# Optimization experiments

Measured on AMD Instinct MI355X. Metric: run time of the kernel, lower is better.

## Reference

```python
import jax, jax.numpy as jnp
import numpy as np

N_NODES = 100000

def gcn_conv(x, row, col, w, W, b, n):
    # PyG GCNConv with edge weights: add self-loops, symmetric normalization.
    loop = jnp.arange(n)
    r = jnp.concatenate([row, loop])
    c = jnp.concatenate([col, loop])
    ew = jnp.concatenate([w, jnp.ones((n,), dtype=x.dtype)])
    deg = jax.ops.segment_sum(ew, c, num_segments=n)          # [N]
    dinv = jnp.where(deg > 0, jax.lax.rsqrt(deg), 0.0)
    norm = dinv[r] * ew * dinv[c]                              # [E+N]
    h = x @ W                                                  # [N, C]
    msg = norm[:, None] * h[r]                                 # [E+N, C]
    out = jax.ops.segment_sum(msg, c, num_segments=n)          # [N, C]
    return out + b

def setup_inputs() -> dict:
    key = jax.random.key(0)
    ks = jax.random.split(key, 9)
    n, F, H, O = N_NODES, 128, 128, 64  # H = 2*out_channels
    E = 1600000
    x = jax.random.normal(ks[0], (n, F), dtype=jnp.float32)
    edge_index = jax.random.randint(ks[1], (2, E), 0, n, dtype=jnp.int64)
    edge_attr = jax.random.uniform(ks[2], (E,), dtype=jnp.float32)
    s = 1.0 / np.sqrt(F)
    W1 = jax.random.uniform(ks[3], (F, H), jnp.float32, -s, s)
    b1 = jnp.zeros((H,), jnp.float32)
    s2 = 1.0 / np.sqrt(H)
    Wmu = jax.random.uniform(ks[4], (H, O), jnp.float32, -s2, s2)
    bmu = jnp.zeros((O,), jnp.float32)
    Wls = jax.random.uniform(ks[5], (H, O), jnp.float32, -s2, s2)
    bls = jnp.zeros((O,), jnp.float32)
    return {"x": x, "edge_index": edge_index, "edge_attr": edge_attr,
            "W1": W1, "b1": b1, "Wmu": Wmu, "bmu": bmu, "Wls": Wls, "bls": bls}

def reference(x, edge_index, edge_attr, W1, b1, Wmu, bmu, Wls, bls):
    n = x.shape[0]
    row, col = edge_index[0], edge_index[1]
    h = jax.nn.relu(gcn_conv(x, row, col, edge_attr, W1, b1, n))
    mu = gcn_conv(h, row, col, edge_attr, Wmu, bmu, n)
    logstd = gcn_conv(h, row, col, edge_attr, Wls, bls, n)
    return (mu, logstd)
```

## Files before the change

### kernel.cpp

```cpp
#include <hip/hip_runtime.h>
#include <math.h>


#define SCAN_B 512

typedef __attribute__((ext_vector_type(8))) short bf16x8;
typedef __attribute__((ext_vector_type(4))) float f32x4;

__device__ __forceinline__ unsigned short f2bf_rne(float f) {
  unsigned int u = __float_as_uint(f);
  u += 0x7FFFu + ((u >> 16) & 1u);
  return (unsigned short)(u >> 16);
}

__device__ __forceinline__ float bf2f(unsigned short h) {
  return __uint_as_float(((unsigned int)h) << 16);
}

__device__ __forceinline__ unsigned int pack2(unsigned short a, unsigned short b) {
  return (unsigned int)a | ((unsigned int)b << 16);
}

__global__ void init_cnt(int* __restrict__ cnt, int n) {
  int i = blockIdx.x * blockDim.x + threadIdx.x;
  if (i < n) cnt[i] = 0;
}

__global__ void hist_rank(const int* __restrict__ col, int* __restrict__ cnt,
                          int* __restrict__ rank, int E) {
  int e = blockIdx.x * blockDim.x + threadIdx.x;
  if (e < E) rank[e] = atomicAdd(&cnt[col[e]], 1);
}

__global__ void scan_blocks(const int* __restrict__ in, int* __restrict__ out,
                            int* __restrict__ bsum, int n) {
  __shared__ int s[SCAN_B];
  int gid = blockIdx.x * SCAN_B + threadIdx.x;
  int v = (gid < n) ? in[gid] : 0;
  s[threadIdx.x] = v;
  __syncthreads();
  for (int off = 1; off < SCAN_B; off <<= 1) {
    int t = (threadIdx.x >= off) ? s[threadIdx.x - off] : 0;
    __syncthreads();
    s[threadIdx.x] += t;
    __syncthreads();
  }
  if (gid < n) out[gid] = s[threadIdx.x] - v;
  if (bsum && threadIdx.x == SCAN_B - 1) bsum[blockIdx.x] = s[SCAN_B - 1];
}

__global__ void add_offsets(int* __restrict__ row_ptr, const int* __restrict__ bsum_ex,
                            int n, int E) {
  int i = blockIdx.x * blockDim.x + threadIdx.x;
  if (i < n) row_ptr[i] += bsum_ex[i >> 9];
  if (i == 0) row_ptr[n] = E;
}

__global__ void scatter_edges(const int* __restrict__ row, const int* __restrict__ col,
                              const float* __restrict__ w,
                              const int* __restrict__ row_ptr,
                              const int* __restrict__ rank,
                              int2* __restrict__ csr, int E) {
  int e = blockIdx.x * blockDim.x + threadIdx.x;
  if (e >= E) return;
  int pos = row_ptr[col[e]] + rank[e];
  csr[pos] = make_int2(row[e], __float_as_int(w[e]));
}

__global__ void deg_dinv(const int* __restrict__ row_ptr, const int2* __restrict__ csr,
                         float* __restrict__ dinv, int n) {
  int i = blockIdx.x * blockDim.x + threadIdx.x;
  if (i >= n) return;
  float s = 1.0f;
  int end = row_ptr[i + 1];
  for (int p = row_ptr[i]; p < end; ++p) s += __int_as_float(csr[p].y);
  dinv[i] = 1.0f / sqrtf(s);
}

__global__ void prep_wt(const float* __restrict__ Wsrc,
                        unsigned short* __restrict__ wt_hi,
                        unsigned short* __restrict__ wt_lo) {
  int i = blockIdx.x * blockDim.x + threadIdx.x;
  if (i >= 128 * 128) return;
  int n = i & 127, k = i >> 7;
  float f = Wsrc[(size_t)k * 128 + n];
  unsigned short h = f2bf_rne(f);
  unsigned short l = f2bf_rne(f - bf2f(h));
  wt_hi[(size_t)n * 128 + k] = h;
  wt_lo[(size_t)n * 128 + k] = l;
}

__global__ void prep_wcat_t(const float* __restrict__ Wmu, const float* __restrict__ Wls,
                            const float* __restrict__ bmu, const float* __restrict__ bls,
                            unsigned short* __restrict__ wt_hi,
                            unsigned short* __restrict__ wt_lo,
                            float* __restrict__ bcat) {
  int i = blockIdx.x * blockDim.x + threadIdx.x;
  if (i >= 128 * 128) return;
  int n = i & 127, k = i >> 7;
  float f = (n < 64) ? Wmu[(size_t)k * 64 + n] : Wls[(size_t)k * 64 + (n - 64)];
  unsigned short h = f2bf_rne(f);
  unsigned short l = f2bf_rne(f - bf2f(h));
  wt_hi[(size_t)n * 128 + k] = h;
  wt_lo[(size_t)n * 128 + k] = l;
  if (i < 128) bcat[i] = (i < 64) ? bmu[i] : bls[i - 64];
}

__global__ __launch_bounds__(256) void gemm_mfma(
    const float* __restrict__ A,
    const unsigned short* __restrict__ WtHi, const unsigned short* __restrict__ WtLo,
    const float* __restrict__ bias, const float* __restrict__ rowscale,
    float* __restrict__ C0, float* __restrict__ C1,
    unsigned short* __restrict__ Cbf, int split, int M) {
  __shared__ uint4 sAhi[1024];
  __shared__ uint4 sAlo[1024];
  __shared__ uint4 sWhi[1024];
  __shared__ uint4 sWlo[1024];

  int tid = threadIdx.x;
  int lane = tid & 63, wid = tid >> 6;
  int wave_r = (wid >> 1) * 64, wave_c = (wid & 1) * 64;
  int lrow = lane & 15, lkb = lane >> 4;
  int rowBase = blockIdx.x * 128;

  f32x4 acc[4][4];
#pragma unroll
  for (int mr = 0; mr < 4; ++mr)
#pragma unroll
    for (int nc = 0; nc < 4; ++nc) acc[mr][nc] = (f32x4){0.f, 0.f, 0.f, 0.f};

  const uint4* WtHi4 = (const uint4*)WtHi;
  const uint4* WtLo4 = (const uint4*)WtLo;

  for (int kt = 0; kt < 128; kt += 64) {
    __syncthreads();
#pragma unroll
    for (int j = 0; j < 4; ++j) {
      int g = tid + 256 * j;
      int c = g >> 3, k8 = g & 7;
      int slot = k8 ^ (c & 7);
      sWhi[c * 8 + slot] = WtHi4[c * 16 + (kt >> 3) + k8];
      sWlo[c * 8 + slot] = WtLo4[c * 16 + (kt >> 3) + k8];
    }
#pragma unroll
    for (int j = 0; j < 4; ++j) {
      int g = tid + 256 * j;
      int r = g >> 3, k8 = g & 7;
      int grow = rowBase + r;
      float4 v0 = make_float4(0.f, 0.f, 0.f, 0.f);
      float4 v1 = v0;
      if (grow < M) {
        const float4* Ar = (const float4*)(A + (size_t)grow * 128 + kt);
        v0 = Ar[k8 * 2];
        v1 = Ar[k8 * 2 + 1];
      }
      float f[8] = {v0.x, v0.y, v0.z, v0.w, v1.x, v1.y, v1.z, v1.w};
      unsigned short h[8], l[8];
#pragma unroll
      for (int q = 0; q < 8; ++q) {
        h[q] = f2bf_rne(f[q]);
        l[q] = f2bf_rne(f[q] - bf2f(h[q]));
      }
      int slot = k8 ^ (r & 7);
      sAhi[r * 8 + slot] = make_uint4(pack2(h[0], h[1]), pack2(h[2], h[3]),
                                      pack2(h[4], h[5]), pack2(h[6], h[7]));
      sAlo[r * 8 + slot] = make_uint4(pack2(l[0], l[1]), pack2(l[2], l[3]),
                                      pack2(l[4], l[5]), pack2(l[6], l[7]));
    }
    __syncthreads();
#pragma unroll
    for (int ks = 0; ks < 2; ++ks) {
      bf16x8 ah[4], al[4], bh[4], bl[4];
#pragma unroll
      for (int mr = 0; mr < 4; ++mr) {
        int r = wave_r + mr * 16 + lrow;
        int slot = (ks * 4 + lkb) ^ (r & 7);
        ah[mr] = *(const bf16x8*)&sAhi[r * 8 + slot];
        al[mr] = *(const bf16x8*)&sAlo[r * 8 + slot];
      }
#pragma unroll
      for (int nc = 0; nc < 4; ++nc) {
        int c = wave_c + nc * 16 + lrow;
        int slot = (ks * 4 + lkb) ^ (c & 7);
        bh[nc] = *(const bf16x8*)&sWhi[c * 8 + slot];
        bl[nc] = *(const bf16x8*)&sWlo[c * 8 + slot];
      }
#pragma unroll
      for (int mr = 0; mr < 4; ++mr)
#pragma unroll
        for (int nc = 0; nc < 4; ++nc) {
          acc[mr][nc] = __builtin_amdgcn_mfma_f32_16x16x32_bf16(
              ah[mr], bh[nc], acc[mr][nc], 0, 0, 0);
          acc[mr][nc] = __builtin_amdgcn_mfma_f32_16x16x32_bf16(
              al[mr], bh[nc], acc[mr][nc], 0, 0, 0);
          acc[mr][nc] = __builtin_amdgcn_mfma_f32_16x16x32_bf16(
              ah[mr], bl[nc], acc[mr][nc], 0, 0, 0);
        }
    }
  }

#pragma unroll
  for (int mr = 0; mr < 4; ++mr) {
    int Rb = rowBase + wave_r + mr * 16 + lkb * 4;
    float sc[4];
#pragma unroll
    for (int reg = 0; reg < 4; ++reg)
      sc[reg] = (rowscale && (Rb + reg) < M) ? rowscale[Rb + reg] : 1.0f;
#pragma unroll
    for (int nc = 0; nc < 4; ++nc) {
      int c = wave_c + nc * 16 + lrow;
      float bb = bias ? bias[c] : 0.f;
      f32x4 v = acc[mr][nc];
#pragma unroll
      for (int reg = 0; reg < 4; ++reg) {
        int R = Rb + reg;
        if (R >= M) continue;
        float val = v[reg] * sc[reg] + bb;
        if (Cbf) Cbf[(size_t)R * 128 + c] = f2bf_rne(val);
        if (C0) {
          if (c < split) C0[(size_t)R * split + c] = val;
          else           C1[(size_t)R * split + (c - split)] = val;
        }
      }
    }
  }
}

__global__ __launch_bounds__(256) void aggregate(
    const ushort4* __restrict__ hin, const int* __restrict__ row_ptr,
    const int2* __restrict__ csr, const float* __restrict__ dinv,
    const float4* __restrict__ bias4, ushort4* __restrict__ hout_bf,
    float4* __restrict__ hout_f4, int n, int do_relu, int scale_out) {
  int node = blockIdx.x * 8 + (threadIdx.x >> 5);
  if (node >= n) return;
  int t = threadIdx.x & 31;
  int beg = row_ptr[node], end = row_ptr[node + 1];
  ushort4 hs = hin[(size_t)node * 32 + t];
  float4 acc = make_float4(bf2f(hs.x), bf2f(hs.y), bf2f(hs.z), bf2f(hs.w));
  int p = beg;
  for (; p + 4 <= end; p += 4) {
    int2 e0 = csr[p + 0];
    int2 e1 = csr[p + 1];
    int2 e2 = csr[p + 2];
    int2 e3 = csr[p + 3];
    ushort4 h0 = hin[(size_t)e0.x * 32 + t];
    ushort4 h1 = hin[(size_t)e1.x * 32 + t];
    ushort4 h2 = hin[(size_t)e2.x * 32 + t];
    ushort4 h3 = hin[(size_t)e3.x * 32 + t];
    float w0 = __int_as_float(e0.y), w1 = __int_as_float(e1.y);
    float w2 = __int_as_float(e2.y), w3 = __int_as_float(e3.y);
    acc.x = fmaf(w0, bf2f(h0.x), acc.x); acc.y = fmaf(w0, bf2f(h0.y), acc.y);
    acc.z = fmaf(w0, bf2f(h0.z), acc.z); acc.w = fmaf(w0, bf2f(h0.w), acc.w);
    acc.x = fmaf(w1, bf2f(h1.x), acc.x); acc.y = fmaf(w1, bf2f(h1.y), acc.y);
    acc.z = fmaf(w1, bf2f(h1.z), acc.z); acc.w = fmaf(w1, bf2f(h1.w), acc.w);
    acc.x = fmaf(w2, bf2f(h2.x), acc.x); acc.y = fmaf(w2, bf2f(h2.y), acc.y);
    acc.z = fmaf(w2, bf2f(h2.z), acc.z); acc.w = fmaf(w2, bf2f(h2.w), acc.w);
    acc.x = fmaf(w3, bf2f(h3.x), acc.x); acc.y = fmaf(w3, bf2f(h3.y), acc.y);
    acc.z = fmaf(w3, bf2f(h3.z), acc.z); acc.w = fmaf(w3, bf2f(h3.w), acc.w);
  }
  for (; p < end; ++p) {
    int2 e = csr[p];
    ushort4 hv = hin[(size_t)e.x * 32 + t];
    float wv = __int_as_float(e.y);
    acc.x = fmaf(wv, bf2f(hv.x), acc.x); acc.y = fmaf(wv, bf2f(hv.y), acc.y);
    acc.z = fmaf(wv, bf2f(hv.z), acc.z); acc.w = fmaf(wv, bf2f(hv.w), acc.w);
  }
  float dc = dinv[node];
  float4 val = make_float4(dc * acc.x, dc * acc.y, dc * acc.z, dc * acc.w);
  if (bias4) {
    float4 b = bias4[t];
    val.x += b.x; val.y += b.y; val.z += b.z; val.w += b.w;
  }
  if (do_relu) {
    val.x = fmaxf(val.x, 0.f); val.y = fmaxf(val.y, 0.f);
    val.z = fmaxf(val.z, 0.f); val.w = fmaxf(val.w, 0.f);
  }
  if (scale_out) {
    val.x *= dc; val.y *= dc; val.z *= dc; val.w *= dc;
  }
  size_t o = (size_t)node * 32 + t;
  if (hout_bf) {
    ushort4 ov;
    ov.x = f2bf_rne(val.x); ov.y = f2bf_rne(val.y);
    ov.z = f2bf_rne(val.z); ov.w = f2bf_rne(val.w);
    hout_bf[o] = ov;
  }
  if (hout_f4) hout_f4[o] = val;
}

extern "C" void kernel_launch(void* const* d_in, const int* in_sizes, int n_in,
                              void* d_out, int out_size, void* d_ws, size_t ws_size,
                              hipStream_t stream) {
  const float* x   = (const float*)d_in[0];
  const int*   ei  = (const int*)d_in[1];
  const float* ea  = (const float*)d_in[2];
  const float* W1  = (const float*)d_in[3];
  const float* b1  = (const float*)d_in[4];
  const float* Wmu = (const float*)d_in[5];
  const float* bmu = (const float*)d_in[6];
  const float* Wls = (const float*)d_in[7];
  const float* bls = (const float*)d_in[8];
  const int N = in_sizes[0] / 128;
  const int E = in_sizes[2];
  const int* row = ei;
  const int* col = ei + E;

  char* p = (char*)d_ws;
  auto alloc = [&](size_t bytes) -> void* {
    void* r = (void*)p;
    p += (bytes + 255) & ~(size_t)255;
    return r;
  };
  float* dinv    = (float*)alloc((size_t)N * 4);
  int*   cnt     = (int*)alloc((size_t)N * 4);
  int*   row_ptr = (int*)alloc((size_t)(N + 1) * 4);
  int*   bsum    = (int*)alloc(1024 * 4);
  int*   bsum_ex = (int*)alloc(1024 * 4);
  unsigned short* w1t_hi = (unsigned short*)alloc(128 * 128 * 2);
  unsigned short* w1t_lo = (unsigned short*)alloc(128 * 128 * 2);
  unsigned short* wct_hi = (unsigned short*)alloc(128 * 128 * 2);
  unsigned short* wct_lo = (unsigned short*)alloc(128 * 128 * 2);
  float* bcat    = (float*)alloc(128 * 4);
  int2*  csr     = (int2*)alloc((size_t)E * 8);
  float* bufA    = (float*)alloc((size_t)N * 128 * 4);
  unsigned short* bufB = (unsigned short*)alloc((size_t)N * 128 * 2);
  unsigned short* bufC = (unsigned short*)alloc((size_t)N * 128 * 2);
  int*   rank    = (int*)bufA;

  float* out_mu = (float*)d_out;
  float* out_ls = out_mu + (size_t)N * 64;

  int nbN = (N + 255) / 256;
  int nbE = (E + 255) / 256;
  int NB  = (N + SCAN_B - 1) / SCAN_B;

  init_cnt<<<nbN, 256, 0, stream>>>(cnt, N);
  hist_rank<<<nbE, 256, 0, stream>>>(col, cnt, rank, E);
  prep_wt<<<64, 256, 0, stream>>>(W1, w1t_hi, w1t_lo);
  prep_wcat_t<<<64, 256, 0, stream>>>(Wmu, Wls, bmu, bls, wct_hi, wct_lo, bcat);
  scan_blocks<<<NB, SCAN_B, 0, stream>>>(cnt, row_ptr, bsum, N);
  scan_blocks<<<1, SCAN_B, 0, stream>>>(bsum, bsum_ex, nullptr, NB);
  add_offsets<<<nbN, 256, 0, stream>>>(row_ptr, bsum_ex, N, E);
  scatter_edges<<<nbE, 256, 0, stream>>>(row, col, ea, row_ptr, rank, csr, E);
  deg_dinv<<<nbN, 256, 0, stream>>>(row_ptr, csr, dinv, N);

  int gblocks = (N + 127) / 128;
  int ablocks = (N + 7) / 8;
  gemm_mfma<<<gblocks, 256, 0, stream>>>(x, w1t_hi, w1t_lo, nullptr, dinv,
                                         nullptr, nullptr, bufB, 128, N);
  aggregate<<<ablocks, 256, 0, stream>>>((const ushort4*)bufB, row_ptr, csr, dinv,
                                         (const float4*)b1, (ushort4*)bufC,
                                         nullptr, N, 1, 1);
  aggregate<<<ablocks, 256, 0, stream>>>((const ushort4*)bufC, row_ptr, csr, dinv,
                                         nullptr, nullptr, (float4*)bufA, N, 0, 0);
  gemm_mfma<<<gblocks, 256, 0, stream>>>(bufA, wct_hi, wct_lo, bcat, nullptr,
                                         out_mu, out_ls, nullptr, 64, N);
}
```

Baseline: 331.2 us.

## Build CSR via two-level bucket partition with shared-memory atomics

Replaces the global-atomic counting sort (per-edge atomicAdd on node counts, multi-level scan, random scatter) with a two-pass radix-style partition. Edges are first bucketed by col>>8 using shared-memory histograms and a per-block scan, then each bucket is sorted by its low 8 bits in a per-bucket kernel that writes row_ptr and the CSR. The goal is to avoid contended global atomics and the scattered global writes of the old path. In exchange it adds an extra pass over the edges and relies on N fitting in 17 bits and at most 512 buckets. Edge order within a node also becomes nondeterministic, which can change float summation order.

Result: faster. 283.6 us (-14.4%).

```diff
diff --git a/kernel.cpp b/kernel.cpp
--- a/kernel.cpp
+++ b/kernel.cpp
@@ -2,7 +2,7 @@
 #include <math.h>
 
 
-#define SCAN_B 512
+#define NBLK 1024
 
 typedef __attribute__((ext_vector_type(8))) short bf16x8;
 typedef __attribute__((ext_vector_type(4))) float f32x4;
@@ -21,50 +21,114 @@
   return (unsigned int)a | ((unsigned int)b << 16);
 }
 
-__global__ void init_cnt(int* __restrict__ cnt, int n) {
-  int i = blockIdx.x * blockDim.x + threadIdx.x;
-  if (i < n) cnt[i] = 0;
-}
-
-__global__ void hist_rank(const int* __restrict__ col, int* __restrict__ cnt,
-                          int* __restrict__ rank, int E) {
-  int e = blockIdx.x * blockDim.x + threadIdx.x;
-  if (e < E) rank[e] = atomicAdd(&cnt[col[e]], 1);
-}
-
-__global__ void scan_blocks(const int* __restrict__ in, int* __restrict__ out,
-                            int* __restrict__ bsum, int n) {
-  __shared__ int s[SCAN_B];
-  int gid = blockIdx.x * SCAN_B + threadIdx.x;
-  int v = (gid < n) ? in[gid] : 0;
+
+__global__ __launch_bounds__(256) void hist_coarse(const int* __restrict__ col,
+                                                   int* __restrict__ G,
+                                                   int E, int nbuck, int epb) {
+  __shared__ int h[512];
+  int blk = blockIdx.x;
+  for (int i = threadIdx.x; i < nbuck; i += 256) h[i] = 0;
+  __syncthreads();
+  int beg = blk * epb;
+  int end = min(beg + epb, E);
+  for (int p = beg + threadIdx.x; p < end; p += 256)
+    atomicAdd(&h[col[p] >> 8], 1);
+  __syncthreads();
+  for (int i = threadIdx.x; i < nbuck; i += 256)
+    G[(size_t)i * NBLK + blk] = h[i];
+}
+
+__global__ __launch_bounds__(1024) void scan_bucket(int* __restrict__ G,
+                                                    int* __restrict__ tot) {
+  __shared__ int s[NBLK];
+  int b = blockIdx.x;
+  int v = G[(size_t)b * NBLK + threadIdx.x];
   s[threadIdx.x] = v;
   __syncthreads();
-  for (int off = 1; off < SCAN_B; off <<= 1) {
+  for (int off = 1; off < NBLK; off <<= 1) {
     int t = (threadIdx.x >= off) ? s[threadIdx.x - off] : 0;
     __syncthreads();
     s[threadIdx.x] += t;
     __syncthreads();
   }
-  if (gid < n) out[gid] = s[threadIdx.x] - v;
-  if (bsum && threadIdx.x == SCAN_B - 1) bsum[blockIdx.x] = s[SCAN_B - 1];
-}
-
-__global__ void add_offsets(int* __restrict__ row_ptr, const int* __restrict__ bsum_ex,
-                            int n, int E) {
-  int i = blockIdx.x * blockDim.x + threadIdx.x;
-  if (i < n) row_ptr[i] += bsum_ex[i >> 9];
-  if (i == 0) row_ptr[n] = E;
-}
-
-__global__ void scatter_edges(const int* __restrict__ row, const int* __restrict__ col,
-                              const float* __restrict__ w,
-                              const int* __restrict__ row_ptr,
-                              const int* __restrict__ rank,
-                              int2* __restrict__ csr, int E) {
-  int e = blockIdx.x * blockDim.x + threadIdx.x;
-  if (e >= E) return;
-  int pos = row_ptr[col[e]] + rank[e];
-  csr[pos] = make_int2(row[e], __float_as_int(w[e]));
+  G[(size_t)b * NBLK + threadIdx.x] = s[threadIdx.x] - v;
+  if (threadIdx.x == NBLK - 1) tot[b] = s[NBLK - 1];
+}
+
+__global__ __launch_bounds__(512) void scan_start(const int* __restrict__ tot,
+                                                  int* __restrict__ start,
+                                                  int* __restrict__ row_ptr,
+                                                  int nbuck, int N, int E) {
+  __shared__ int s[512];
+  int v = (threadIdx.x < nbuck) ? tot[threadIdx.x] : 0;
+  s[threadIdx.x] = v;
+  __syncthreads();
+  for (int off = 1; off < 512; off <<= 1) {
+    int t = (threadIdx.x >= off) ? s[threadIdx.x - off] : 0;
+    __syncthreads();
+    s[threadIdx.x] += t;
+    __syncthreads();
+  }
+  if (threadIdx.x < nbuck) start[threadIdx.x] = s[threadIdx.x] - v;
+  if (threadIdx.x == 511) start[nbuck] = s[511];
+  if (threadIdx.x == 0) row_ptr[N] = E;
+}
+
+__global__ __launch_bounds__(256) void partition_edges(
+    const int* __restrict__ row, const int* __restrict__ col,
+    const float* __restrict__ w, const int* __restrict__ G,
+    const int* __restrict__ start, int2* __restrict__ part,
+    int E, int nbuck, int epb) {
+  __shared__ int cur[512];
+  int blk = blockIdx.x;
+  for (int i = threadIdx.x; i < nbuck; i += 256)
+    cur[i] = start[i] + G[(size_t)i * NBLK + blk];
+  __syncthreads();
+  int beg = blk * epb;
+  int end = min(beg + epb, E);
+  for (int p = beg + threadIdx.x; p < end; p += 256) {
+    int c = col[p];
+    int pos = atomicAdd(&cur[c >> 8], 1);
+    part[pos] = make_int2(row[p] | ((c & 255) << 17),
+                          __float_as_int(w[p]));
+  }
+}
+
+__global__ __launch_bounds__(256) void build_fine(const int* __restrict__ start,
+                                                  const int2* __restrict__ part,
+                                                  int* __restrict__ row_ptr,
+                                                  int2* __restrict__ csr,
+                                                  int N) {
+  __shared__ int hist[256];
+  __shared__ int sc[256];
+  __shared__ int cur[256];
+  int b = blockIdx.x;
+  int ebeg = start[b], eend = start[b + 1];
+  hist[threadIdx.x] = 0;
+  __syncthreads();
+  for (int p = ebeg + threadIdx.x; p < eend; p += 256)
+    atomicAdd(&hist[(part[p].x >> 17) & 255], 1);
+  __syncthreads();
+  int v = hist[threadIdx.x];
+  sc[threadIdx.x] = v;
+  __syncthreads();
+  for (int off = 1; off < 256; off <<= 1) {
+    int t = (threadIdx.x >= off) ? sc[threadIdx.x - off] : 0;
+    __syncthreads();
+    sc[threadIdx.x] += t;
+    __syncthreads();
+  }
+  int ex = sc[threadIdx.x] - v;
+  int node = b * 256 + threadIdx.x;
+  if (node < N) row_ptr[node] = ebeg + ex;
+  cur[threadIdx.x] = ebeg + ex;
+  __syncthreads();
+  for (int p = ebeg + threadIdx.x; p < eend; p += 256) {
+    int2 r = part[p];
+    int cl = (r.x >> 17) & 255;
+    int pos = atomicAdd(&cur[cl], 1);
+    csr[pos] = make_int2(r.x & 0x1FFFF, r.y);
+  }
 }
 
 __global__ void deg_dinv(const int* __restrict__ row_ptr, const int2* __restrict__ csr,
@@ -312,10 +376,7 @@
     return r;
   };
   float* dinv    = (float*)alloc((size_t)N * 4);
-  int*   cnt     = (int*)alloc((size_t)N * 4);
   int*   row_ptr = (int*)alloc((size_t)(N + 1) * 4);
-  int*   bsum    = (int*)alloc(1024 * 4);
-  int*   bsum_ex = (int*)alloc(1024 * 4);
   unsigned short* w1t_hi = (unsigned short*)alloc(128 * 128 * 2);
   unsigned short* w1t_lo = (unsigned short*)alloc(128 * 128 * 2);
   unsigned short* wct_hi = (unsigned short*)alloc(128 * 128 * 2);
@@ -325,23 +386,28 @@
   float* bufA    = (float*)alloc((size_t)N * 128 * 4);
   unsigned short* bufB = (unsigned short*)alloc((size_t)N * 128 * 2);
   unsigned short* bufC = (unsigned short*)alloc((size_t)N * 128 * 2);
-  int*   rank    = (int*)bufA;
+
+  int2* part  = (int2*)bufA;
+  int*  G     = (int*)bufB;
+  int*  tot   = (int*)((char*)bufB + (size_t)512 * NBLK * 4);
+  int*  start = tot + 512;
 
   float* out_mu = (float*)d_out;
   float* out_ls = out_mu + (size_t)N * 64;
 
+  const int nbuck = (N + 255) >> 8;
+  const int epb   = (E + NBLK - 1) / NBLK;
   int nbN = (N + 255) / 256;
-  int nbE = (E + 255) / 256;
-  int NB  = (N + SCAN_B - 1) / SCAN_B;
-
-  init_cnt<<<nbN, 256, 0, stream>>>(cnt, N);
-  hist_rank<<<nbE, 256, 0, stream>>>(col, cnt, rank, E);
+
   prep_wt<<<64, 256, 0, stream>>>(W1, w1t_hi, w1t_lo);
   prep_wcat_t<<<64, 256, 0, stream>>>(Wmu, Wls, bmu, bls, wct_hi, wct_lo, bcat);
-  scan_blocks<<<NB, SCAN_B, 0, stream>>>(cnt, row_ptr, bsum, N);
-  scan_blocks<<<1, SCAN_B, 0, stream>>>(bsum, bsum_ex, nullptr, NB);
-  add_offsets<<<nbN, 256, 0, stream>>>(row_ptr, bsum_ex, N, E);
-  scatter_edges<<<nbE, 256, 0, stream>>>(row, col, ea, row_ptr, rank, csr, E);
+
+  hist_coarse<<<NBLK, 256, 0, stream>>>(col, G, E, nbuck, epb);
+  scan_bucket<<<nbuck, NBLK, 0, stream>>>(G, tot);
+  scan_start<<<1, 512, 0, stream>>>(tot, start, row_ptr, nbuck, N, E);
+  partition_edges<<<NBLK, 256, 0, stream>>>(row, col, ea, G, start, part,
+                                            E, nbuck, epb);
+  build_fine<<<nbuck, 256, 0, stream>>>(start, part, row_ptr, csr, N);
   deg_dinv<<<nbN, 256, 0, stream>>>(row_ptr, csr, dinv, N);
 
   int gblocks = (N + 127) / 128;
```
